# Optimization experiments

Measured on AMD Instinct MI355X. Metric: run time of the kernel, lower is better.

Reference implementation:

```python
import jax, jax.numpy as jnp
import numpy as np

B, T, D_DATA = 256, 256, 16
H, WD, ODE, S = 128, 256, 32, 8  # hidden, width, ode_size, scaling_factor

# Tsit5 tableau (5th-order solution; FSAL stage k7 has b7=0 and is error-only)
A21 = 0.161
A31, A32 = -0.008480655492356989, 0.335480655492357
A41, A42, A43 = 2.8971530571054935, -6.359448489975075, 4.3622954328695815
A51, A52, A53, A54 = 5.325864828439257, -11.748883564062828, 7.4955393428898365, -0.09249506636175525
A61, A62, A63, A64, A65 = 5.86145544294642, -12.92096931784711, 8.159367898576159, -0.071584973281401, -0.028269050394068383
B1, B2, B3, B4, B5, B6 = 0.09646076681806523, 0.01, 0.4798896504144996, 1.379008574103742, -3.290069515436081, 2.324710524099774

def _mask_enc(d, s):
    m = np.ones((s * d, d), np.float32)
    for i in range(d):
        m[(i + 1) * s:, i] = 0.0
    return jnp.asarray(m)

def _mask_dec(d, s):
    m = np.zeros((d, d * s), np.float32)
    for i in range(d):
        m[i, i * s:] = 1.0
    return jnp.asarray(m)

def setup_inputs():
    key = jax.random.key(0)
    ks = jax.random.split(key, 24)
    g = lambda k, shp, fan: jax.random.normal(k, shp, jnp.float32) / np.float32(np.sqrt(fan))
    triu = jnp.asarray(np.triu(np.ones((S * ODE, S * ODE), np.float32)))
    return {
        "ts": jnp.linspace(0.0, 5.0, T).astype(jnp.float32),
        "yi": jax.random.normal(ks[0], (B, T, D_DATA), jnp.float32),
        "gru_wih": g(ks[1], (3 * H, D_DATA), D_DATA),
        "gru_whh": g(ks[2], (3 * H, H), H),
        "gru_b": g(ks[3], (3 * H,), H),
        "gru_bn": g(ks[4], (H,), H),
        "h2o_W1": g(ks[5], (WD, H), H), "h2o_b1": g(ks[6], (WD,), H),
        "h2o_W2": g(ks[7], (WD, WD), WD), "h2o_b2": g(ks[8], (WD,), WD),
        "h2o_W3": g(ks[9], (ODE, WD), WD), "h2o_b3": g(ks[10], (ODE,), WD),
        "cf_W0": g(ks[11], (S * ODE, ODE), ODE) * _mask_enc(ODE, S),
        "cf_W1": g(ks[12], (S * ODE, S * ODE), S * ODE) * triu,
        "cf_W2": g(ks[13], (S * ODE, S * ODE), S * ODE) * triu,
        "cf_Wout": g(ks[14], (ODE, S * ODE), S * ODE) * _mask_dec(ODE, S),
        "o2d_W1": g(ks[15], (WD, ODE), ODE), "o2d_b1": g(ks[16], (WD,), ODE),
        "o2d_W2": g(ks[17], (WD, WD), WD), "o2d_b2": g(ks[18], (WD,), WD),
        "o2d_W3": g(ks[19], (D_DATA, WD), WD), "o2d_b3": g(ks[20], (D_DATA,), WD),
    }

def reference(ts, yi, gru_wih, gru_whh, gru_b, gru_bn,
              h2o_W1, h2o_b1, h2o_W2, h2o_b2, h2o_W3, h2o_b3,
              cf_W0, cf_W1, cf_W2, cf_Wout,
              o2d_W1, o2d_b1, o2d_W2, o2d_b2, o2d_W3, o2d_b3):
    # --- GRU encoder over reversed sequence, batched over B ---
    def gru_step(h, x):
        ig = x @ gru_wih.T + gru_b          # [B, 3H]
        hg = h @ gru_whh.T                  # [B, 3H]
        ir, iz, ic = jnp.split(ig, 3, axis=-1)
        hr, hz, hn = jnp.split(hg, 3, axis=-1)
        r = jax.nn.sigmoid(ir + hr)
        z = jax.nn.sigmoid(iz + hz)
        n = jnp.tanh(ic + r * (hn + gru_bn))
        return n + z * (h - n), None
    h0 = jnp.zeros((yi.shape[0], gru_whh.shape[1]), yi.dtype)
    hidden, _ = jax.lax.scan(gru_step, h0, jnp.transpose(yi, (1, 0, 2))[::-1])
    # --- hidden -> ODE initial state (MLP depth 2, tanh) ---
    y0 = jnp.tanh(hidden @ h2o_W1.T + h2o_b1)
    y0 = jnp.tanh(y0 @ h2o_W2.T + h2o_b2)
    y0 = y0 @ h2o_W3.T + h2o_b3             # [B, ODE]
    # --- causal vector field (autonomous, bias-free masked layers) ---
    def f(y):
        x = jnp.tanh(y @ cf_W0.T)
        x = jnp.tanh(x @ cf_W1.T)
        x = jnp.tanh(x @ cf_W2.T)
        return x @ cf_Wout.T
    # --- Tsit5: one explicit step per save interval ---
    def tsit5_step(y, h):
        k1 = f(y)
        k2 = f(y + h * (A21 * k1))
        k3 = f(y + h * (A31 * k1 + A32 * k2))
        k4 = f(y + h * (A41 * k1 + A42 * k2 + A43 * k3))
        k5 = f(y + h * (A51 * k1 + A52 * k2 + A53 * k3 + A54 * k4))
        k6 = f(y + h * (A61 * k1 + A62 * k2 + A63 * k3 + A64 * k4 + A65 * k5))
        ynew = y + h * (B1 * k1 + B2 * k2 + B3 * k3 + B4 * k4 + B5 * k5 + B6 * k6)
        return ynew, ynew
    _, ys_tail = jax.lax.scan(tsit5_step, y0, ts[1:] - ts[:-1])
    ys = jnp.concatenate([y0[None], ys_tail], axis=0)    # [T, B, ODE]
    # --- ODE -> data MLP (identity activation) ---
    out = ys @ o2d_W1.T + o2d_b1
    out = out @ o2d_W2.T + o2d_b2
    out = out @ o2d_W3.T + o2d_b3
    return jnp.transpose(out, (1, 0, 2))                 # [B, T, D_DATA]
```

## Files before the change

### kernel.cpp

```cpp
#include <hip/hip_runtime.h>


typedef unsigned short u16;
typedef unsigned int u32;
typedef _Float16 f16;
typedef __attribute__((ext_vector_type(8))) _Float16 f16x8;
typedef __attribute__((ext_vector_type(4))) float f32x4;

#define MFMA16(A, B, C) __builtin_amdgcn_mfma_f32_16x16x32_f16((A), (B), (C), 0, 0, 0)

__device__ __forceinline__ u16 f16bits(f16 h) { union { f16 f; u16 u; } c; c.f = h; return c.u; }
__device__ __forceinline__ f16 bitsf16(u16 u) { union { f16 f; u16 u; } c; c.u = u; return c.f; }
__device__ __forceinline__ void split(float v, f16& hi, f16& lo) {
    hi = (f16)v;
    lo = (f16)(v - (float)hi);
}
__device__ __forceinline__ u32 packf16(float v) {
    f16 hi, lo;
    split(v, hi, lo);
    return (u32)f16bits(hi) | ((u32)f16bits(lo) << 16);
}
__device__ __forceinline__ float fsig(float x) { return 1.0f / (1.0f + __expf(-x)); }
__device__ __forceinline__ float ftanh(float x) {
    float e = __expf(2.0f * x);
    return 1.0f - 2.0f / (e + 1.0f);
}

constexpr float cAc[6][6] = {
    {0.161f, 0.f, 0.f, 0.f, 0.f, 0.f},
    {-0.008480655492356989f, 0.335480655492357f, 0.f, 0.f, 0.f, 0.f},
    {2.8971530571054935f, -6.359448489975075f, 4.3622954328695815f, 0.f, 0.f, 0.f},
    {5.325864828439257f, -11.748883564062828f, 7.4955393428898365f, -0.09249506636175525f, 0.f, 0.f},
    {5.86145544294642f, -12.92096931784711f, 8.159367898576159f, -0.071584973281401f, -0.028269050394068383f, 0.f},
    {0.09646076681806523f, 0.01f, 0.4798896504144996f, 1.379008574103742f, -3.290069515436081f, 2.324710524099774f}};

__global__ __launch_bounds__(512, 2) void gru_h2o_kernel(
    const float* __restrict__ yi,
    const float* __restrict__ wih,
    const float* __restrict__ whh,
    const float* __restrict__ gb,
    const float* __restrict__ gbn,
    const float* __restrict__ hW1, const float* __restrict__ hb1,
    const float* __restrict__ hW2, const float* __restrict__ hb2,
    const float* __restrict__ hW3, const float* __restrict__ hb3,
    u32* __restrict__ ys)
{
    const int b = blockIdx.x;
    const int tid = threadIdx.x;
    const int wave = tid >> 6;
    const int lane = tid & 63;
    const int quad = lane >> 4;
    const int col = lane & 15;
    const int j = wave * 16 + col;

    __shared__ alignas(16) f16 s_a[2][4][160];
    __shared__ float s_h[128];
    __shared__ float s_t[256];

    const f32x4 ZC = {0.f, 0.f, 0.f, 0.f};

    f16x8 wf[3][5][2];
#pragma unroll
    for (int tt = 0; tt < 3; ++tt) {
        const int n = (wave + tt * 8) * 16 + col;
#pragma unroll
        for (int kk = 0; kk < 5; ++kk) {
            const int k0 = kk * 32 + quad * 8;
            float w8[8];
            if (k0 < 16) {
#pragma unroll
                for (int jj = 0; jj < 8; ++jj) w8[jj] = wih[n * 16 + k0 + jj];
            } else if (k0 < 144) {
#pragma unroll
                for (int jj = 0; jj < 8; ++jj) w8[jj] = whh[n * 128 + (k0 - 16) + jj];
            } else {
#pragma unroll
                for (int jj = 0; jj < 8; ++jj) w8[jj] = 0.0f;
            }
            f16x8 hi, lo;
#pragma unroll
            for (int jj = 0; jj < 8; ++jj) {
                f16 h, l;
                split(w8[jj], h, l);
                hi[jj] = h;
                lo[jj] = l;
            }
            wf[tt][kk][0] = hi;
            wf[tt][kk][1] = lo;
        }
    }

    const float b_r = gb[j];
    const float b_z = gb[128 + j];
    const float b_c = gb[256 + j];
    const float b_n = gbn[j];

    for (int i = tid; i < 2 * 4 * 160; i += 512) ((f16*)s_a)[i] = (f16)0.0f;
    __syncthreads();
    if (tid < 16) {
        const float xv = yi[(size_t)b * 4096 + 255 * 16 + tid];
        f16 hi, lo;
        split(xv, hi, lo);
        s_a[0][0][tid] = hi;
        s_a[0][1][tid] = lo;
        s_a[0][2][tid] = hi;
        s_a[0][3][tid] = lo;
    }
    __syncthreads();

    float h = 0.0f;
#pragma unroll 1
    for (int ti = 0; ti < 256; ++ti) {
        const int p = ti & 1;
        const int np = 1 - p;
        float xnext = 0.0f;
        if (tid < 16 && ti < 255) xnext = yi[(size_t)b * 4096 + (254 - ti) * 16 + tid];

        f32x4 a0 = ZC, a1 = ZC, a2 = ZC;
#pragma unroll
        for (int kk = 0; kk < 5; ++kk) {
            const f16x8 a = *(const f16x8*)&s_a[p][col & 3][kk * 32 + quad * 8];
            a0 = MFMA16(a, wf[0][kk][0], a0);
            a0 = MFMA16(a, wf[0][kk][1], a0);
            a1 = MFMA16(a, wf[1][kk][0], a1);
            a1 = MFMA16(a, wf[1][kk][1], a1);
            a2 = MFMA16(a, wf[2][kk][0], a2);
            a2 = MFMA16(a, wf[2][kk][1], a2);
        }
        {
            const float sum_r = a0[0] + a0[1];
            const float sum_z = a1[0] + a1[1];
            const float sum_c = a2[0] + a2[1];
            const float icc = a2[2] + a2[3];
            const float r = fsig(sum_r + b_r);
            const float z = fsig(sum_z + b_z);
            const float ic = icc + b_c;
            const float hn = (sum_c - icc) + b_n;
            const float nn = ftanh(ic + r * hn);
            h = nn + z * (h - nn);
        }
        if (quad == 0) {
            f16 hh, hl;
            split(h, hh, hl);
            s_a[np][0][16 + j] = hh;
            s_a[np][1][16 + j] = hl;
        }
        if (tid < 16 && ti < 255) {
            f16 hi, lo;
            split(xnext, hi, lo);
            s_a[np][0][tid] = hi;
            s_a[np][1][tid] = lo;
            s_a[np][2][tid] = hi;
            s_a[np][3][tid] = lo;
        }
        __syncthreads();
    }

    if (quad == 0) s_h[j] = h;
    __syncthreads();

    float a1v = 0.0f;
    if (tid < 256) {
        a1v = hb1[tid];
        const float* w = hW1 + (size_t)tid * 128;
#pragma unroll 8
        for (int p = 0; p < 128; ++p) a1v += w[p] * s_h[p];
        a1v = ftanh(a1v);
        s_t[tid] = a1v;
    }
    __syncthreads();
    float a2v = 0.0f;
    if (tid < 256) {
        a2v = hb2[tid];
        const float* w = hW2 + (size_t)tid * 256;
#pragma unroll 8
        for (int p = 0; p < 256; ++p) a2v += w[p] * s_t[p];
        a2v = ftanh(a2v);
    }
    __syncthreads();
    if (tid < 256) s_t[tid] = a2v;
    __syncthreads();
    if (tid < 32) {
        float a3 = hb3[tid];
        const float* w = hW3 + (size_t)tid * 256;
#pragma unroll 8
        for (int p = 0; p < 256; ++p) a3 += w[p] * s_t[p];
        ys[(size_t)b * 32 + tid] = packf16(a3);
    }
}

__global__ __launch_bounds__(512, 2) void ode_kernel(
    const float* __restrict__ ts,
    const float* __restrict__ W0,
    const float* __restrict__ W1,
    const float* __restrict__ W2,
    const float* __restrict__ Wo,
    u32* __restrict__ ys)
{
    const int b = blockIdx.x;
    const int tid = threadIdx.x;
    const int wave = tid >> 6;
    const int lane = tid & 63;
    const int quad = lane >> 4;
    const int col = lane & 15;
    const int half = quad >> 1;
    const int hl = quad & 1;
    const int cidx = col + half * 16;

    __shared__ alignas(16) f16 s_x0[2][256];
    __shared__ alignas(16) f16 s_x1[2][256];
    __shared__ alignas(16) f16 s_x2w[8][2][32];
    __shared__ alignas(16) f16 s_yw[8][2][32];
    __shared__ float s_part[8][32];
    __shared__ float s_ts[256];

    if (tid < 256) s_ts[tid] = ts[tid];

    const f32x4 ZC = {0.f, 0.f, 0.f, 0.f};

    f16x8 w0f[2][2], w1f[2][8], w2f[2][8], wof[2][2];
#pragma unroll
    for (int tt = 0; tt < 2; ++tt) {
        const int n = (wave * 2 + tt) * 16 + col;
        {
            f16x8 hi, lo;
#pragma unroll
            for (int jj = 0; jj < 8; ++jj) {
                f16 h, l;
                split(W0[n * 32 + quad * 8 + jj], h, l);
                hi[jj] = h;
                lo[jj] = l;
            }
            w0f[tt][0] = hi;
            w0f[tt][1] = lo;
        }
#pragma unroll
        for (int kk = 0; kk < 8; ++kk) {
            f16x8 h1, h2;
#pragma unroll
            for (int jj = 0; jj < 8; ++jj) {
                h1[jj] = (f16)W1[n * 256 + kk * 32 + quad * 8 + jj];
                h2[jj] = (f16)W2[n * 256 + kk * 32 + quad * 8 + jj];
            }
            w1f[tt][kk] = h1;
            w2f[tt][kk] = h2;
        }
        {
            const int n3 = tt * 16 + col;
            f16x8 hi, lo;
#pragma unroll
            for (int jj = 0; jj < 8; ++jj) {
                f16 h, l;
                split(Wo[n3 * 256 + wave * 32 + quad * 8 + jj], h, l);
                hi[jj] = h;
                lo[jj] = l;
            }
            wof[tt][0] = hi;
            wof[tt][1] = lo;
        }
    }

    float ybase;
    {
        const u32 p = ys[(size_t)b * 32 + cidx];
        const f16 yh = bitsf16((u16)(p & 0xffffu));
        const f16 yl = bitsf16((u16)(p >> 16));
        ybase = (float)yh + (float)yl;
        s_yw[wave][hl][cidx] = hl ? yl : yh;
    }
    float k_hist[6];
#pragma unroll
    for (int i = 0; i < 6; ++i) k_hist[i] = 0.0f;

    __syncthreads();

    auto do_L0_x0 = [&]() {
        const f16x8 a = *(const f16x8*)&s_yw[wave][col & 1][quad * 8];
        f32x4 aA = MFMA16(a, w0f[0][0], ZC);
        aA = MFMA16(a, w0f[0][1], aA);
        f32x4 aB = MFMA16(a, w0f[1][0], ZC);
        aB = MFMA16(a, w0f[1][1], aB);
        const float e = half ? (aB[0] + aB[1]) : (aA[0] + aA[1]);
        const float x = ftanh(e);
        const f16 xh = (f16)x;
        s_x0[hl][(wave * 2 + half) * 16 + col] = hl ? (f16)(x - (float)xh) : xh;
    };

    do_L0_x0();
    __syncthreads();

#pragma unroll 1
    for (int t = 0; t < 255; ++t) {
        const float hstep = s_ts[t + 1] - s_ts[t];
#pragma unroll
        for (int s = 0; s < 6; ++s) {
            {
                f32x4 e0 = ZC, e1 = ZC, o0 = ZC, o1 = ZC;
#pragma unroll
                for (int kk = 0; kk < 8; kk += 2) {
                    const f16x8 ae = *(const f16x8*)&s_x0[col & 1][kk * 32 + quad * 8];
                    const f16x8 ao = *(const f16x8*)&s_x0[col & 1][(kk + 1) * 32 + quad * 8];
                    e0 = MFMA16(ae, w1f[0][kk], e0);
                    e1 = MFMA16(ae, w1f[1][kk], e1);
                    o0 = MFMA16(ao, w1f[0][kk + 1], o0);
                    o1 = MFMA16(ao, w1f[1][kk + 1], o1);
                }
                const float e = half ? (e1[0] + e1[1] + o1[0] + o1[1])
                                     : (e0[0] + e0[1] + o0[0] + o0[1]);
                const float x = ftanh(e);
                const f16 xh = (f16)x;
                s_x1[hl][(wave * 2 + half) * 16 + col] = hl ? (f16)(x - (float)xh) : xh;
            }
            __syncthreads();
            {
                f32x4 e0 = ZC, e1 = ZC, o0 = ZC, o1 = ZC;
#pragma unroll
                for (int kk = 0; kk < 8; kk += 2) {
                    const f16x8 ae = *(const f16x8*)&s_x1[col & 1][kk * 32 + quad * 8];
                    const f16x8 ao = *(const f16x8*)&s_x1[col & 1][(kk + 1) * 32 + quad * 8];
                    e0 = MFMA16(ae, w2f[0][kk], e0);
                    e1 = MFMA16(ae, w2f[1][kk], e1);
                    o0 = MFMA16(ao, w2f[0][kk + 1], o0);
                    o1 = MFMA16(ao, w2f[1][kk + 1], o1);
                }
                const float e = half ? (e1[0] + e1[1] + o1[0] + o1[1])
                                     : (e0[0] + e0[1] + o0[0] + o0[1]);
                const float x = ftanh(e);
                const f16 xh = (f16)x;
                s_x2w[wave][hl][half * 16 + col] = hl ? (f16)(x - (float)xh) : xh;
                const f16x8 a = *(const f16x8*)&s_x2w[wave][col & 1][quad * 8];
                f32x4 p0 = MFMA16(a, wof[0][0], ZC);
                p0 = MFMA16(a, wof[0][1], p0);
                f32x4 p1 = MFMA16(a, wof[1][0], ZC);
                p1 = MFMA16(a, wof[1][1], p1);
                if (quad == 0) s_part[wave][col] = p0[0] + p0[1];
                if (quad == 1) s_part[wave][16 + col] = p1[0] + p1[1];
            }
            __syncthreads();
            {
                float kv = 0.0f;
#pragma unroll
                for (int p = 0; p < 8; ++p) kv += s_part[p][cidx];
                k_hist[s] = kv;
                float sum = 0.0f;
#pragma unroll
                for (int i = 0; i < 6; ++i)
                    if (i <= s) sum += cAc[s][i] * k_hist[i];
                const float v = ybase + hstep * sum;
                if (s == 5) {
                    ybase = v;
                    if (wave == 0 && !hl)
                        ys[((size_t)(t + 1) * 256 + b) * 32 + cidx] = packf16(v);
                }
                const f16 vh = (f16)v;
                s_yw[wave][hl][cidx] = hl ? (f16)(v - (float)vh) : vh;
                do_L0_x0();
            }
            __syncthreads();
        }
    }
}

__global__ __launch_bounds__(256, 1) void o2d_kernel(
    const u32* __restrict__ ys,
    const float* __restrict__ W1, const float* __restrict__ b1,
    const float* __restrict__ W2, const float* __restrict__ b2,
    const float* __restrict__ W3, const float* __restrict__ b3,
    float* __restrict__ out)
{
    const int r0 = blockIdx.x * 16;
    const int tid = threadIdx.x;
    const int wave = tid >> 6;
    const int lane = tid & 63;
    const int quad = lane >> 4;
    const int col = lane & 15;

    __shared__ alignas(16) f16 s_a[2][16][32];
    __shared__ alignas(16) f16 s_x[2][2][16][264];
    __shared__ float s_part[4][16][16];

    const f32x4 ZC = {0.f, 0.f, 0.f, 0.f};

    f16x8 w1f[4][2], w2f[4][8][2], w3f[2][2];
    float b1r[4], b2r[4];
#pragma unroll
    for (int tt = 0; tt < 4; ++tt) {
        const int n = (wave * 4 + tt) * 16 + col;
        b1r[tt] = b1[n];
        b2r[tt] = b2[n];
        {
            f16x8 hi, lo;
#pragma unroll
            for (int jj = 0; jj < 8; ++jj) {
                f16 h, l;
                split(W1[n * 32 + quad * 8 + jj], h, l);
                hi[jj] = h;
                lo[jj] = l;
            }
            w1f[tt][0] = hi;
            w1f[tt][1] = lo;
        }
#pragma unroll
        for (int kk = 0; kk < 8; ++kk) {
            f16x8 hi, lo;
#pragma unroll
            for (int jj = 0; jj < 8; ++jj) {
                f16 h, l;
                split(W2[n * 256 + kk * 32 + quad * 8 + jj], h, l);
                hi[jj] = h;
                lo[jj] = l;
            }
            w2f[tt][kk][0] = hi;
            w2f[tt][kk][1] = lo;
        }
    }
#pragma unroll
    for (int c = 0; c < 2; ++c) {
        const int kk = wave * 2 + c;
        f16x8 hi, lo;
#pragma unroll
        for (int jj = 0; jj < 8; ++jj) {
            f16 h, l;
            split(W3[col * 256 + kk * 32 + quad * 8 + jj], h, l);
            hi[jj] = h;
            lo[jj] = l;
        }
        w3f[c][0] = hi;
        w3f[c][1] = lo;
    }

    {
        const int row = tid >> 4;
        const int k2 = (tid & 15) * 2;
        const u32 p0 = ys[(size_t)(r0 + row) * 32 + k2];
        const u32 p1 = ys[(size_t)(r0 + row) * 32 + k2 + 1];
        s_a[0][row][k2] = bitsf16((u16)(p0 & 0xffffu));
        s_a[0][row][k2 + 1] = bitsf16((u16)(p1 & 0xffffu));
        s_a[1][row][k2] = bitsf16((u16)(p0 >> 16));
        s_a[1][row][k2 + 1] = bitsf16((u16)(p1 >> 16));
    }
    __syncthreads();

    f32x4 acc[4];
#pragma unroll
    for (int tt = 0; tt < 4; ++tt) acc[tt] = ZC;
#pragma unroll
    for (int hl = 0; hl < 2; ++hl) {
        const f16x8 a = *(const f16x8*)&s_a[hl][col][quad * 8];
#pragma unroll
        for (int bl = 0; bl < 2; ++bl)
#pragma unroll
            for (int tt = 0; tt < 4; ++tt) acc[tt] = MFMA16(a, w1f[tt][bl], acc[tt]);
    }
#pragma unroll
    for (int tt = 0; tt < 4; ++tt) {
        const int n = (wave * 4 + tt) * 16 + col;
#pragma unroll
        for (int rg = 0; rg < 4; ++rg) {
            const int row = quad * 4 + rg;
            const float v = acc[tt][rg] + b1r[tt];
            f16 hi, lo;
            split(v, hi, lo);
            s_x[0][0][row][n] = hi;
            s_x[0][1][row][n] = lo;
        }
    }
    __syncthreads();
#pragma unroll
    for (int tt = 0; tt < 4; ++tt) acc[tt] = ZC;
#pragma unroll
    for (int kk = 0; kk < 8; ++kk) {
#pragma unroll
        for (int hl = 0; hl < 2; ++hl) {
            const f16x8 a = *(const f16x8*)&s_x[0][hl][col][kk * 32 + quad * 8];
#pragma unroll
            for (int bl = 0; bl < 2; ++bl)
#pragma unroll
                for (int tt = 0; tt < 4; ++tt) acc[tt] = MFMA16(a, w2f[tt][kk][bl], acc[tt]);
        }
    }
#pragma unroll
    for (int tt = 0; tt < 4; ++tt) {
        const int n = (wave * 4 + tt) * 16 + col;
#pragma unroll
        for (int rg = 0; rg < 4; ++rg) {
            const int row = quad * 4 + rg;
            const float v = acc[tt][rg] + b2r[tt];
            f16 hi, lo;
            split(v, hi, lo);
            s_x[1][0][row][n] = hi;
            s_x[1][1][row][n] = lo;
        }
    }
    __syncthreads();
    f32x4 a3 = ZC;
#pragma unroll
    for (int c = 0; c < 2; ++c) {
        const int kk = wave * 2 + c;
#pragma unroll
        for (int hl = 0; hl < 2; ++hl) {
            const f16x8 a = *(const f16x8*)&s_x[1][hl][col][kk * 32 + quad * 8];
#pragma unroll
            for (int bl = 0; bl < 2; ++bl) a3 = MFMA16(a, w3f[c][bl], a3);
        }
    }
#pragma unroll
    for (int rg = 0; rg < 4; ++rg) s_part[wave][quad * 4 + rg][col] = a3[rg];
    __syncthreads();
    {
        const int row = tid >> 4;
        const int cc = tid & 15;
        const float v = s_part[0][row][cc] + s_part[1][row][cc] + s_part[2][row][cc] +
                        s_part[3][row][cc] + b3[cc];
        const int r = r0 + row;
        const int bb = r & 255;
        const int tt2 = r >> 8;
        out[((size_t)bb * 256 + tt2) * 16 + cc] = v;
    }
}

extern "C" void kernel_launch(void* const* d_in, const int* in_sizes, int n_in,
                              void* d_out, int out_size, void* d_ws, size_t ws_size,
                              hipStream_t stream) {
    (void)in_sizes; (void)n_in; (void)out_size; (void)ws_size;
    const float* ts      = (const float*)d_in[0];
    const float* yi      = (const float*)d_in[1];
    const float* gru_wih = (const float*)d_in[2];
    const float* gru_whh = (const float*)d_in[3];
    const float* gru_b   = (const float*)d_in[4];
    const float* gru_bn  = (const float*)d_in[5];
    const float* h2o_W1  = (const float*)d_in[6];
    const float* h2o_b1  = (const float*)d_in[7];
    const float* h2o_W2  = (const float*)d_in[8];
    const float* h2o_b2  = (const float*)d_in[9];
    const float* h2o_W3  = (const float*)d_in[10];
    const float* h2o_b3  = (const float*)d_in[11];
    const float* cf_W0   = (const float*)d_in[12];
    const float* cf_W1   = (const float*)d_in[13];
    const float* cf_W2   = (const float*)d_in[14];
    const float* cf_Wout = (const float*)d_in[15];
    const float* o2d_W1  = (const float*)d_in[16];
    const float* o2d_b1  = (const float*)d_in[17];
    const float* o2d_W2  = (const float*)d_in[18];
    const float* o2d_b2  = (const float*)d_in[19];
    const float* o2d_W3  = (const float*)d_in[20];
    const float* o2d_b3  = (const float*)d_in[21];

    u32* ys = (u32*)d_ws;

    gru_h2o_kernel<<<256, 512, 0, stream>>>(yi, gru_wih, gru_whh, gru_b, gru_bn,
                                            h2o_W1, h2o_b1, h2o_W2, h2o_b2, h2o_W3, h2o_b3, ys);
    ode_kernel<<<256, 512, 0, stream>>>(ts, cf_W0, cf_W1, cf_W2, cf_Wout, ys);
    o2d_kernel<<<4096, 256, 0, stream>>>(ys, o2d_W1, o2d_b1, o2d_W2, o2d_b2,
                                         o2d_W3, o2d_b3, (float*)d_out);
}
```

Baseline: 2.252 ms.

## Fold layer-0 weights into output projection and track preactivation in latent space

```diff
diff --git a/kernel.cpp b/kernel.cpp
--- a/kernel.cpp
+++ b/kernel.cpp
@@ -206,34 +206,76 @@
     const int half = quad >> 1;
     const int hl = quad & 1;
     const int cidx = col + half * 16;
-
-    __shared__ alignas(16) f16 s_x0[2][256];
-    __shared__ alignas(16) f16 s_x1[2][256];
-    __shared__ alignas(16) f16 s_x2w[8][2][32];
-    __shared__ alignas(16) f16 s_yw[8][2][32];
+    const int nown = (wave * 2 + half) * 16 + col;
+
+    __shared__ alignas(16) f16 s_x0[2][288];
+    __shared__ alignas(16) f16 s_x1[2][288];
+    __shared__ alignas(16) f16 s_x2[2][288];
     __shared__ float s_part[8][32];
     __shared__ float s_ts[256];
+    __shared__ float s_w0[256 * 33];
+    __shared__ alignas(16) float s_wout[32 * 256];
 
     if (tid < 256) s_ts[tid] = ts[tid];
+    for (int i = tid; i < 32 * 256; i += 512) s_wout[i] = Wo[i];
+    for (int i = tid; i < 256 * 32; i += 512) s_w0[(i >> 5) * 33 + (i & 31)] = W0[i];
+
+    float ybase;
+    {
+        const u32 p = ys[(size_t)b * 32 + cidx];
+        ybase = (float)bitsf16((u16)(p & 0xffffu)) + (float)bitsf16((u16)(p >> 16));
+    }
+    if (tid < 32) {
+        const u32 p = ys[(size_t)b * 32 + tid];
+        s_part[0][tid] = (float)bitsf16((u16)(p & 0xffffu)) + (float)bitsf16((u16)(p >> 16));
+    }
+    __syncthreads();
 
     const f32x4 ZC = {0.f, 0.f, 0.f, 0.f};
-
-    f16x8 w0f[2][2], w1f[2][8], w2f[2][8], wof[2][2];
+    const int n0 = (wave * 2 + 0) * 16 + col;
+    const int n1 = (wave * 2 + 1) * 16 + col;
+
+    f16x8 wFf[2][8];
+#pragma unroll 1
+    for (int kk = 0; kk < 8; ++kk) {
+        float a0[8], a1[8];
+#pragma unroll
+        for (int jj = 0; jj < 8; ++jj) { a0[jj] = 0.f; a1[jj] = 0.f; }
+#pragma unroll 8
+        for (int m = 0; m < 32; ++m) {
+            const float w00 = s_w0[n0 * 33 + m];
+            const float w01 = s_w0[n1 * 33 + m];
+            const float* wp = &s_wout[m * 256 + kk * 32 + quad * 8];
+#pragma unroll
+            for (int jj = 0; jj < 8; ++jj) {
+                const float wv = wp[jj];
+                a0[jj] += w00 * wv;
+                a1[jj] += w01 * wv;
+            }
+        }
+        f16x8 f0, f1;
+#pragma unroll
+        for (int jj = 0; jj < 8; ++jj) { f0[jj] = (f16)a0[jj]; f1[jj] = (f16)a1[jj]; }
+        wFf[0][kk] = f0;
+        wFf[1][kk] = f1;
+    }
+
+    float G_base;
+    {
+        float gb0 = 0.f, gb1 = 0.f;
+#pragma unroll 8
+        for (int m = 0; m < 32; ++m) {
+            const float y0m = s_part[0][m];
+            gb0 += s_w0[n0 * 33 + m] * y0m;
+            gb1 += s_w0[n1 * 33 + m] * y0m;
+        }
+        G_base = half ? gb1 : gb0;
+    }
+
+    f16x8 w1f[2][8], w2f[2][8], wof[2][2];
 #pragma unroll
     for (int tt = 0; tt < 2; ++tt) {
         const int n = (wave * 2 + tt) * 16 + col;
-        {
-            f16x8 hi, lo;
-#pragma unroll
-            for (int jj = 0; jj < 8; ++jj) {
-                f16 h, l;
-                split(W0[n * 32 + quad * 8 + jj], h, l);
-                hi[jj] = h;
-                lo[jj] = l;
-            }
-            w0f[tt][0] = hi;
-            w0f[tt][1] = lo;
-        }
 #pragma unroll
         for (int kk = 0; kk < 8; ++kk) {
             f16x8 h1, h2;
@@ -260,33 +302,16 @@
         }
     }
 
-    float ybase;
     {
-        const u32 p = ys[(size_t)b * 32 + cidx];
-        const f16 yh = bitsf16((u16)(p & 0xffffu));
-        const f16 yl = bitsf16((u16)(p >> 16));
-        ybase = (float)yh + (float)yl;
-        s_yw[wave][hl][cidx] = hl ? yl : yh;
-    }
-    float k_hist[6];
-#pragma unroll
-    for (int i = 0; i < 6; ++i) k_hist[i] = 0.0f;
-
-    __syncthreads();
-
-    auto do_L0_x0 = [&]() {
-        const f16x8 a = *(const f16x8*)&s_yw[wave][col & 1][quad * 8];
-        f32x4 aA = MFMA16(a, w0f[0][0], ZC);
-        aA = MFMA16(a, w0f[0][1], aA);
-        f32x4 aB = MFMA16(a, w0f[1][0], ZC);
-        aB = MFMA16(a, w0f[1][1], aB);
-        const float e = half ? (aB[0] + aB[1]) : (aA[0] + aA[1]);
-        const float x = ftanh(e);
+        const float x = ftanh(G_base);
         const f16 xh = (f16)x;
-        s_x0[hl][(wave * 2 + half) * 16 + col] = hl ? (f16)(x - (float)xh) : xh;
-    };
-
-    do_L0_x0();
+        s_x0[hl][nown] = hl ? (f16)(x - (float)xh) : xh;
+    }
+
+    float k_hist[6], g_hist[6];
+#pragma unroll
+    for (int i = 0; i < 6; ++i) { k_hist[i] = 0.0f; g_hist[i] = 0.0f; }
+
     __syncthreads();
 
 #pragma unroll 1
@@ -309,7 +334,7 @@
                                      : (e0[0] + e0[1] + o0[0] + o0[1]);
                 const float x = ftanh(e);
                 const f16 xh = (f16)x;
-                s_x1[hl][(wave * 2 + half) * 16 + col] = hl ? (f16)(x - (float)xh) : xh;
+                s_x1[hl][nown] = hl ? (f16)(x - (float)xh) : xh;
             }
             __syncthreads();
             {
@@ -327,8 +352,8 @@
                                      : (e0[0] + e0[1] + o0[0] + o0[1]);
                 const float x = ftanh(e);
                 const f16 xh = (f16)x;
-                s_x2w[wave][hl][half * 16 + col] = hl ? (f16)(x - (float)xh) : xh;
-                const f16x8 a = *(const f16x8*)&s_x2w[wave][col & 1][quad * 8];
+                s_x2[hl][nown] = hl ? (f16)(x - (float)xh) : xh;
+                const f16x8 a = *(const f16x8*)&s_x2[col & 1][wave * 32 + quad * 8];
                 f32x4 p0 = MFMA16(a, wof[0][0], ZC);
                 p0 = MFMA16(a, wof[0][1], p0);
                 f32x4 p1 = MFMA16(a, wof[1][0], ZC);
@@ -341,20 +366,37 @@
                 float kv = 0.0f;
 #pragma unroll
                 for (int p = 0; p < 8; ++p) kv += s_part[p][cidx];
+                f32x4 e0 = ZC, e1 = ZC, o0 = ZC, o1 = ZC;
+#pragma unroll
+                for (int kk = 0; kk < 8; kk += 2) {
+                    const f16x8 ae = *(const f16x8*)&s_x2[col & 1][kk * 32 + quad * 8];
+                    const f16x8 ao = *(const f16x8*)&s_x2[col & 1][(kk + 1) * 32 + quad * 8];
+                    e0 = MFMA16(ae, wFf[0][kk], e0);
+                    e1 = MFMA16(ae, wFf[1][kk], e1);
+                    o0 = MFMA16(ao, wFf[0][kk + 1], o0);
+                    o1 = MFMA16(ao, wFf[1][kk + 1], o1);
+                }
+                const float g = half ? (e1[0] + e1[1] + o1[0] + o1[1])
+                                     : (e0[0] + e0[1] + o0[0] + o0[1]);
                 k_hist[s] = kv;
-                float sum = 0.0f;
+                g_hist[s] = g;
+                float gsum = 0.0f;
 #pragma unroll
                 for (int i = 0; i < 6; ++i)
-                    if (i <= s) sum += cAc[s][i] * k_hist[i];
-                const float v = ybase + hstep * sum;
+                    if (i <= s) gsum += cAc[s][i] * g_hist[i];
+                const float Garg = G_base + hstep * gsum;
                 if (s == 5) {
-                    ybase = v;
+                    G_base = Garg;
+                    float ysum = 0.0f;
+#pragma unroll
+                    for (int i = 0; i < 6; ++i) ysum += cAc[5][i] * k_hist[i];
+                    ybase += hstep * ysum;
                     if (wave == 0 && !hl)
-                        ys[((size_t)(t + 1) * 256 + b) * 32 + cidx] = packf16(v);
+                        ys[((size_t)(t + 1) * 256 + b) * 32 + cidx] = packf16(ybase);
                 }
-                const f16 vh = (f16)v;
-                s_yw[wave][hl][cidx] = hl ? (f16)(v - (float)vh) : vh;
-                do_L0_x0();
+                const float x = ftanh(Garg);
+                const f16 xh = (f16)x;
+                s_x0[hl][nown] = hl ? (f16)(x - (float)xh) : xh;
             }
             __syncthreads();
         }
```

Measured after the change: 7.887 ms. 250% more time.
